# Performance work log

Hardware: AMD Instinct MI355X
Metric: run time of the kernel (lower is better)

The kernel has to match this reference:

```python
import jax, jax.numpy as jnp
import numpy as np

B, T, D, H = 2, 2048, 1024, 16
DH = D // H  # 64


def setup_inputs() -> dict:
    key = jax.random.key(0)
    ks = jax.random.split(key, 11)
    s = 1.0 / np.sqrt(D)
    return {
        "q": jax.random.normal(ks[0], (B, T, D), jnp.float32),
        "k": jax.random.normal(ks[1], (B, T, D), jnp.float32),
        "v": jax.random.normal(ks[2], (B, T, D), jnp.float32),
        "Wq": jax.random.normal(ks[3], (D, D), jnp.float32) * s,
        "bq": jnp.zeros((D,), jnp.float32),
        "Wk": jax.random.normal(ks[4], (D, D), jnp.float32) * s,
        "bk": jnp.zeros((D,), jnp.float32),
        "Wv": jax.random.normal(ks[5], (D, D), jnp.float32) * s,
        "bv": jnp.zeros((D,), jnp.float32),
        "Wo": jax.random.normal(ks[6], (D, D), jnp.float32) * s,
        "bo": jnp.zeros((D,), jnp.float32),
    }


def reference(q, k, v, Wq, bq, Wk, bk, Wv, bv, Wo, bo):
    Bq, Tq, _ = q.shape
    Tk = k.shape[1]
    # projections, split heads: [B, H, T, DH]
    qh = (q @ Wq + bq).reshape(Bq, Tq, H, DH).transpose(0, 2, 1, 3)
    kh = (k @ Wk + bk).reshape(Bq, Tk, H, DH).transpose(0, 2, 1, 3)
    vh = (v @ Wv + bv).reshape(Bq, Tk, H, DH).transpose(0, 2, 1, 3)
    # scores [B, H, Tq, Tk]
    scores = jnp.einsum("bhqd,bhkd->bhqk", qh, kh) / np.sqrt(DH)
    # causal mask with diagonal offset Tk - Tq (matches torch.tril semantics)
    ii = jnp.arange(Tq)[:, None]
    jj = jnp.arange(Tk)[None, :]
    causal = jj <= ii + (Tk - Tq)
    scores = jnp.where(causal, scores, -jnp.inf)
    attn = jax.nn.softmax(scores, axis=-1)
    x = jnp.einsum("bhqk,bhkd->bhqd", attn, vh)  # [B, H, Tq, DH]
    x = x.transpose(0, 2, 1, 3).reshape(Bq, Tq, H * DH)
    return x @ Wo + bo
```

## Files before the change

### kernel.cpp

```cpp
#include <hip/hip_runtime.h>

typedef unsigned short u16;
typedef unsigned int   u32;
typedef __attribute__((ext_vector_type(8)))  short short8;
typedef __attribute__((ext_vector_type(4)))  float f32x4;
typedef __attribute__((ext_vector_type(16))) float f32x16;
typedef __attribute__((ext_vector_type(2)))  u32 uint2v;
typedef __attribute__((ext_vector_type(4)))  u32 uint4v;

#define DEV __device__ __forceinline__

DEV u16 f2bf(float f) {
    u32 u = __builtin_bit_cast(u32, f);
    return (u16)((u + 0x7fffu + ((u >> 16) & 1u)) >> 16);
}
DEV float bf2f(u32 u) { return __builtin_bit_cast(float, u << 16); }
DEV u32 cvtpk(float a, float b) {
    u32 r;
    asm("v_cvt_pk_bf16_f32 %0, %1, %2" : "=v"(r) : "v"(a), "v"(b));
    return r;
}
typedef const __attribute__((address_space(1))) u32 g_u32;
typedef __attribute__((address_space(3))) u32 l_u32;
DEV void gload16(const u16* g, u16* l) {
    __builtin_amdgcn_global_load_lds((g_u32*)g, (l_u32*)l, 16, 0, 0);
}


template<int OMODE>
DEV void gemm_body(const u16* __restrict__ A_, const u16* __restrict__ Bt,
                   const float* __restrict__ bias, float oscale, void* C_) {
    constexpr int Kd = 1024;
    const int m0 = blockIdx.y * 128, n0 = blockIdx.x * 128;
    const int t = threadIdx.x, lane = t & 63, w = t >> 6;
    const int wm = w >> 1, wn = w & 1;
    const int l15 = lane & 15, l4 = lane >> 4;
    __shared__ __align__(16) u16 As[128 * 32];
    __shared__ __align__(16) u16 Bs[128 * 32];
    f32x4 acc[4][4] = {};

    for (int k0 = 0; k0 < Kd; k0 += 32) {
        #pragma unroll
        for (int rnd = 0; rnd < 2; rnd++) {
            int cc = rnd * 256 + t, row = cc >> 2, slot = cc & 3;
            gload16(Bt + (size_t)(n0 + row) * Kd + k0 + slot * 8, Bs + cc * 8);
            gload16(A_ + (size_t)(m0 + row) * Kd + k0 + slot * 8, As + cc * 8);
        }
        __syncthreads();
        short8 af[4], bfr[4];
        #pragma unroll
        for (int i = 0; i < 4; i++) {
            af[i]  = *(const short8*)(As + (wm * 64 + i * 16 + l15) * 32 + l4 * 8);
            bfr[i] = *(const short8*)(Bs + (wn * 64 + i * 16 + l15) * 32 + l4 * 8);
        }
        #pragma unroll
        for (int i = 0; i < 4; i++)
            #pragma unroll
            for (int j = 0; j < 4; j++)
                acc[i][j] = __builtin_amdgcn_mfma_f32_16x16x32_bf16(af[i], bfr[j], acc[i][j], 0, 0, 0);
        __syncthreads();
    }

    #pragma unroll
    for (int i = 0; i < 4; i++) {
        #pragma unroll
        for (int j = 0; j < 4; j++) {
            int col = n0 + wn * 64 + j * 16 + l15;
            int mb  = m0 + wm * 64 + i * 16 + l4 * 4;
            float bv = bias[col];
            if (OMODE == 2) {
                float* C = (float*)C_;
                #pragma unroll
                for (int r = 0; r < 4; r++)
                    C[(size_t)(mb + r) * 1024 + col] = acc[i][j][r] + bv;
            } else if (OMODE == 0) {
                u16* C = (u16*)C_;
                #pragma unroll
                for (int r = 0; r < 4; r++)
                    C[(size_t)(mb + r) * 1024 + col] = f2bf((acc[i][j][r] + bv) * oscale);
            } else if (OMODE == 3) {
                u16* C = (u16*)C_;
                int hh = col >> 6, dd = col & 63;
                int bb = mb >> 11, tt = mb & 2047;
                size_t tile = ((size_t)(bb * 16 + hh) * 64 + (tt >> 5)) * 2048;
                int c = dd >> 4, hi2 = (dd >> 3) & 1, e = dd & 7;
                int lob = tt & 31;
                #pragma unroll
                for (int r = 0; r < 4; r++)
                    C[tile + (size_t)((c * 2 + hi2) * 32 + lob + r) * 8 + e] =
                        f2bf(acc[i][j][r] + bv);
            } else {
                u16* C = (u16*)C_;
                int hh = col >> 6, dd = col & 63;
                int bb = mb >> 11, tt = mb & 2047;
                size_t tile = ((size_t)(bb * 16 + hh) * 64 + (tt >> 5)) * 2048;
                int tin = tt & 31, kc = tin >> 4, hi2 = (tin >> 3) & 1, e0 = tin & 7;
                int c2 = dd >> 5, lo2 = dd & 31;
                size_t off = tile + (size_t)((kc * 2 + c2) * 64 + hi2 * 32 + lo2) * 8 + e0;
                uint2v pp;
                pp[0] = cvtpk(acc[i][j][0] + bv, acc[i][j][1] + bv);
                pp[1] = cvtpk(acc[i][j][2] + bv, acc[i][j][3] + bv);
                *(uint2v*)(C + off) = pp;
            }
        }
    }
}

__global__ __launch_bounds__(256) void k_transw(const float* Wq, const float* Wk,
                                                const float* Wv, const float* Wo, u16* Wt) {
    int z = blockIdx.z;
    const float* W = z == 0 ? Wq : z == 1 ? Wk : z == 2 ? Wv : Wo;
    u16* O = Wt + (size_t)z * 1048576;
    __shared__ float tile[32][33];
    int n0 = blockIdx.x * 32, k0 = blockIdx.y * 32;
    int tx = threadIdx.x, ty = threadIdx.y;
    #pragma unroll
    for (int i = 0; i < 32; i += 8) tile[ty + i][tx] = W[(size_t)(k0 + ty + i) * 1024 + n0 + tx];
    __syncthreads();
    #pragma unroll
    for (int i = 0; i < 32; i += 8) O[(size_t)(n0 + ty + i) * 1024 + k0 + tx] = f2bf(tile[tx][ty + i]);
}

__global__ __launch_bounds__(256) void k_cvt(const float* q, const float* k, const float* v,
                                             u16* Abf) {
    int z = blockIdx.z;
    const float* src = z == 0 ? q : z == 1 ? k : v;
    u16* dst = Abf + (size_t)z * 4194304;
    size_t i = ((size_t)blockIdx.x * 256 + threadIdx.x) * 8;
    float4 a = *(const float4*)(src + i);
    float4 b = *(const float4*)(src + i + 4);
    uint4v o;
    o[0] = cvtpk(a.x, a.y); o[1] = cvtpk(a.z, a.w);
    o[2] = cvtpk(b.x, b.y); o[3] = cvtpk(b.z, b.w);
    *(uint4v*)(dst + i) = o;
}

__global__ __launch_bounds__(256) void k_proj(const u16* Abf, const u16* Wt,
                                              const float* bq, const float* bk,
                                              const float* bv, u16* QKV) {
    int z = blockIdx.z;
    if (z == 2)
        gemm_body<1>(Abf + (size_t)2 * 4194304, Wt + (size_t)2 * 1048576, bv, 1.f,
                     QKV + (size_t)2 * 4194304);
    else if (z == 1)
        gemm_body<3>(Abf + (size_t)4194304, Wt + (size_t)1048576, bk, 1.f,
                     QKV + (size_t)4194304);
    else
        gemm_body<0>(Abf, Wt, bq, 0.125f, QKV);
}

__global__ __launch_bounds__(256) void k_combine(const u16* Xp, const float* Lp, u16* Xc) {
    size_t idx = (size_t)blockIdx.x * 256 + threadIdx.x;
    size_t e = idx * 8;
    int row = (int)(e >> 10), hh = ((int)e & 1023) >> 6;
    float l0 = Lp[(size_t)row * 16 + hh];
    float l1 = Lp[65536 + (size_t)row * 16 + hh];
    float s = 1.0f / (l0 + l1);
    float w0 = l0 * s, w1 = l1 * s;
    uint4v x0 = *(const uint4v*)(Xp + e);
    uint4v x1 = *(const uint4v*)(Xp + (size_t)4194304 + e);
    uint4v o;
    #pragma unroll
    for (int j = 0; j < 4; j++) {
        float a0 = bf2f(x0[j] & 0xffffu) * w0 + bf2f(x1[j] & 0xffffu) * w1;
        float a1 = bf2f(x0[j] >> 16)    * w0 + bf2f(x1[j] >> 16)    * w1;
        o[j] = cvtpk(a0, a1);
    }
    *(uint4v*)(Xc + e) = o;
}

__global__ __launch_bounds__(256) void k_gemm_out(const u16* Xc, const u16* Wt,
                                                  const float* bo, float* out) {
    gemm_body<2>(Xc, Wt, bo, 1.f, out);
}

__global__ __launch_bounds__(256, 3) void k_attn(const u16* __restrict__ Qp,
                                                 const u16* __restrict__ Kp2,
                                                 const u16* __restrict__ Vp2,
                                                 u16* __restrict__ Xp, float* __restrict__ Lp) {
    const int bh = blockIdx.y, b = bh >> 4, h = bh & 15;
    const int t = threadIdx.x, lane = t & 63, w = t >> 6;
    const int lo = lane & 31, hi = lane >> 5;
    const int split = blockIdx.z;
    const int q0w = (int)(gridDim.x - 1 - blockIdx.x) * 128 + w * 32;
    const u16* Qb = Qp + (size_t)(b * 2048) * 1024 + h * 64;
    const u16* Kb = Kp2 + (size_t)bh * 64 * 2048;
    const u16* Vb = Vp2 + (size_t)bh * 64 * 2048;

    short8 qf[4];
    #pragma unroll
    for (int c = 0; c < 4; c++)
        qf[c] = *(const short8*)(Qb + (size_t)(q0w + lo) * 1024 + c * 16 + hi * 8);

    f32x16 O0 = {}, O1 = {};
    float lsum = 0.f;
    const int qg = q0w + lo;
    const int nk = (q0w >> 5) + 1;
    const int c0 = (nk + 1) >> 1;
    const int kbeg = split ? (c0 << 5) : 0;
    const int kend = split ? (nk << 5) : (c0 << 5);

#define LOADKV(KF, VF, kk) do {                                                          \
        const u16* kt_ = Kb + (size_t)((kk) >> 5) * 2048;                                \
        const u16* vt_ = Vb + (size_t)((kk) >> 5) * 2048;                                \
        _Pragma("unroll")                                                                \
        for (int c = 0; c < 4; c++)                                                      \
            KF[c] = *(const short8*)(kt_ + c * 512 + lane * 8);                          \
        _Pragma("unroll")                                                                \
        for (int j = 0; j < 4; j++)                                                      \
            VF[j] = *(const short8*)(vt_ + j * 512 + lane * 8);                          \
    } while (0)

#define COMPUTE(KF, VF, kk) do {                                                          \
        f32x16 S = {};                                                                    \
        _Pragma("unroll")                                                                 \
        for (int c = 0; c < 4; c++)                                                       \
            S = __builtin_amdgcn_mfma_f32_32x32x16_bf16(KF[c], qf[c], S, 0, 0, 0);        \
        const bool diag = ((kk) == q0w);                                                  \
        _Pragma("unroll")                                                                 \
        for (int kc = 0; kc < 2; kc++) {                                                  \
            float p[8];                                                                   \
            _Pragma("unroll")                                                             \
            for (int j = 0; j < 8; j++) {                                                 \
                int r = kc * 8 + j;                                                       \
                float s = S[r];                                                           \
                if (diag) {                                                               \
                    int kg = (kk) + (r & 3) + 8 * (r >> 2) + 4 * hi;                      \
                    s = (kg <= qg) ? s : -1e30f;                                          \
                }                                                                         \
                p[j] = __expf(s);                                                         \
            }                                                                             \
            lsum += (((p[0] + p[1]) + (p[2] + p[3])) + ((p[4] + p[5]) + (p[6] + p[7])));  \
            u32 w0 = cvtpk(p[0], p[1]), w1 = cvtpk(p[2], p[3]);                           \
            u32 w2 = cvtpk(p[4], p[5]), w3 = cvtpk(p[6], p[7]);                           \
            auto r0 = __builtin_amdgcn_permlane32_swap(w0, w2, false, false);             \
            auto r1 = __builtin_amdgcn_permlane32_swap(w1, w3, false, false);             \
            uint4v fw; fw[0] = r0[0]; fw[1] = r1[0]; fw[2] = r0[1]; fw[3] = r1[1];        \
            short8 pf = __builtin_bit_cast(short8, fw);                                   \
            O0 = __builtin_amdgcn_mfma_f32_32x32x16_bf16(pf, VF[kc * 2 + 0], O0, 0, 0, 0);\
            O1 = __builtin_amdgcn_mfma_f32_32x32x16_bf16(pf, VF[kc * 2 + 1], O1, 0, 0, 0);\
        }                                                                                 \
    } while (0)

    if (kbeg < kend) {
        short8 kf0[4], vf0[4], kf1[4], vf1[4];
        LOADKV(kf0, vf0, kbeg);
        int k0 = kbeg;
        while (true) {
            if (k0 + 32 < kend) LOADKV(kf1, vf1, k0 + 32);
            COMPUTE(kf0, vf0, k0);
            k0 += 32;
            if (k0 >= kend) break;
            if (k0 + 32 < kend) LOADKV(kf0, vf0, k0 + 32);
            COMPUTE(kf1, vf1, k0);
            k0 += 32;
            if (k0 >= kend) break;
        }
    }
#undef LOADKV
#undef COMPUTE

    float ltot = lsum + __shfl_xor(lsum, 32, 64);
    u16* Xb = Xp + (size_t)split * 4194304;
    #pragma unroll
    for (int r = 0; r < 16; r++) {
        int qr = (r & 3) + 8 * (r >> 2) + 4 * hi;
        float lt = __shfl(ltot, qr, 64);
        float linv = lt > 0.f ? 1.f / lt : 0.f;
        size_t rowb = (size_t)(b * 2048 + q0w + qr) * 1024 + h * 64;
        Xb[rowb + lo]      = f2bf(O0[r] * linv);
        Xb[rowb + 32 + lo] = f2bf(O1[r] * linv);
    }
    if (hi == 0)
        Lp[(size_t)split * 65536 + (size_t)(b * 2048 + q0w + lo) * 16 + h] = ltot;
}

extern "C" void kernel_launch(void* const* d_in, const int* in_sizes, int n_in,
                              void* d_out, int out_size, void* d_ws, size_t ws_size,
                              hipStream_t stream) {
    (void)in_sizes; (void)n_in; (void)out_size; (void)ws_size;
    const float* q  = (const float*)d_in[0];
    const float* k  = (const float*)d_in[1];
    const float* v  = (const float*)d_in[2];
    const float* Wq = (const float*)d_in[3];
    const float* bq = (const float*)d_in[4];
    const float* Wk = (const float*)d_in[5];
    const float* bk = (const float*)d_in[6];
    const float* Wv = (const float*)d_in[7];
    const float* bv = (const float*)d_in[8];
    const float* Wo = (const float*)d_in[9];
    const float* bo = (const float*)d_in[10];

    u16*   Wt  = (u16*)d_ws;
    u16*   QKV = Wt + (size_t)4 * 1048576;
    u16*   Abf = QKV + (size_t)3 * 4194304;
    u16*   Xp  = Abf;
    u16*   Xc  = Abf + (size_t)2 * 4194304;
    float* Lp  = (float*)(Abf + (size_t)3 * 4194304);

    k_transw<<<dim3(32, 32, 4), dim3(32, 8), 0, stream>>>(Wq, Wk, Wv, Wo, Wt);
    k_cvt<<<dim3(2048, 1, 3), 256, 0, stream>>>(q, k, v, Abf);
    k_proj<<<dim3(8, 32, 3), 256, 0, stream>>>(Abf, Wt, bq, bk, bv, QKV);
    k_attn<<<dim3(16, 32, 2), 256, 0, stream>>>(QKV, QKV + (size_t)4194304,
                                                QKV + (size_t)2 * 4194304, Xp, Lp);
    k_combine<<<2048, 256, 0, stream>>>(Xp, Lp, Xc);
    k_gemm_out<<<dim3(8, 32), 256, 0, stream>>>(Xc, Wt + (size_t)3 * 1048576,
                                                bo, (float*)d_out);
}
```

Before: 139.4 us.

## Pair causal query tiles per wave to balance work and drop split-K combine

Each wave now processes two mirrored 32-row query tiles (p and 63-p), so every wave does the same total number of key tiles under the causal mask. The key/value fragments are loaded once and shared by both tiles. This replaces the two-way key split, so the partial outputs, the Lp row sums and the k_combine kernel are no longer needed. In exchange the grid shrinks from 1024 to 256 blocks, launch bounds are lowered to one block, and register use roughly doubles because of the extra accumulators, which can reduce occupancy and latency hiding.

After: 134.0 us. 1.04x faster.

```diff
diff --git a/kernel.cpp b/kernel.cpp
--- a/kernel.cpp
+++ b/kernel.cpp
@@ -149,60 +149,39 @@
         gemm_body<0>(Abf, Wt, bq, 0.125f, QKV);
 }
 
-__global__ __launch_bounds__(256) void k_combine(const u16* Xp, const float* Lp, u16* Xc) {
-    size_t idx = (size_t)blockIdx.x * 256 + threadIdx.x;
-    size_t e = idx * 8;
-    int row = (int)(e >> 10), hh = ((int)e & 1023) >> 6;
-    float l0 = Lp[(size_t)row * 16 + hh];
-    float l1 = Lp[65536 + (size_t)row * 16 + hh];
-    float s = 1.0f / (l0 + l1);
-    float w0 = l0 * s, w1 = l1 * s;
-    uint4v x0 = *(const uint4v*)(Xp + e);
-    uint4v x1 = *(const uint4v*)(Xp + (size_t)4194304 + e);
-    uint4v o;
-    #pragma unroll
-    for (int j = 0; j < 4; j++) {
-        float a0 = bf2f(x0[j] & 0xffffu) * w0 + bf2f(x1[j] & 0xffffu) * w1;
-        float a1 = bf2f(x0[j] >> 16)    * w0 + bf2f(x1[j] >> 16)    * w1;
-        o[j] = cvtpk(a0, a1);
-    }
-    *(uint4v*)(Xc + e) = o;
-}
-
 __global__ __launch_bounds__(256) void k_gemm_out(const u16* Xc, const u16* Wt,
                                                   const float* bo, float* out) {
     gemm_body<2>(Xc, Wt, bo, 1.f, out);
 }
 
-__global__ __launch_bounds__(256, 3) void k_attn(const u16* __restrict__ Qp,
+__global__ __launch_bounds__(256, 1) void k_attn(const u16* __restrict__ Qp,
                                                  const u16* __restrict__ Kp2,
                                                  const u16* __restrict__ Vp2,
-                                                 u16* __restrict__ Xp, float* __restrict__ Lp) {
+                                                 u16* __restrict__ Xc) {
     const int bh = blockIdx.y, b = bh >> 4, h = bh & 15;
     const int t = threadIdx.x, lane = t & 63, w = t >> 6;
     const int lo = lane & 31, hi = lane >> 5;
-    const int split = blockIdx.z;
-    const int q0w = (int)(gridDim.x - 1 - blockIdx.x) * 128 + w * 32;
+    const int p = blockIdx.x * 4 + w;
+    const int q0a = p * 32, q0b = (63 - p) * 32;
+    const int nka = p + 1, nkb = 64 - p;
     const u16* Qb = Qp + (size_t)(b * 2048) * 1024 + h * 64;
     const u16* Kb = Kp2 + (size_t)bh * 64 * 2048;
     const u16* Vb = Vp2 + (size_t)bh * 64 * 2048;
 
-    short8 qf[4];
+    short8 qfa[4], qfb[4];
     #pragma unroll
-    for (int c = 0; c < 4; c++)
-        qf[c] = *(const short8*)(Qb + (size_t)(q0w + lo) * 1024 + c * 16 + hi * 8);
-
-    f32x16 O0 = {}, O1 = {};
-    float lsum = 0.f;
-    const int qg = q0w + lo;
-    const int nk = (q0w >> 5) + 1;
-    const int c0 = (nk + 1) >> 1;
-    const int kbeg = split ? (c0 << 5) : 0;
-    const int kend = split ? (nk << 5) : (c0 << 5);
-
-#define LOADKV(KF, VF, kk) do {                                                          \
-        const u16* kt_ = Kb + (size_t)((kk) >> 5) * 2048;                                \
-        const u16* vt_ = Vb + (size_t)((kk) >> 5) * 2048;                                \
+    for (int c = 0; c < 4; c++) {
+        qfa[c] = *(const short8*)(Qb + (size_t)(q0a + lo) * 1024 + c * 16 + hi * 8);
+        qfb[c] = *(const short8*)(Qb + (size_t)(q0b + lo) * 1024 + c * 16 + hi * 8);
+    }
+
+    f32x16 Oa0 = {}, Oa1 = {}, Ob0 = {}, Ob1 = {};
+    float lsa = 0.f, lsb = 0.f;
+    const int qga = q0a + lo, qgb = q0b + lo;
+
+#define LOADKV(KF, VF, kt) do {                                                          \
+        const u16* kt_ = Kb + (size_t)(kt) * 2048;                                       \
+        const u16* vt_ = Vb + (size_t)(kt) * 2048;                                       \
         _Pragma("unroll")                                                                \
         for (int c = 0; c < 4; c++)                                                      \
             KF[c] = *(const short8*)(kt_ + c * 512 + lane * 8);                          \
@@ -211,28 +190,24 @@
             VF[j] = *(const short8*)(vt_ + j * 512 + lane * 8);                          \
     } while (0)
 
-#define COMPUTE(KF, VF, kk) do {                                                          \
-        f32x16 S = {};                                                                    \
-        _Pragma("unroll")                                                                 \
-        for (int c = 0; c < 4; c++)                                                       \
-            S = __builtin_amdgcn_mfma_f32_32x32x16_bf16(KF[c], qf[c], S, 0, 0, 0);        \
-        const bool diag = ((kk) == q0w);                                                  \
+#define SMPV(S, O0, O1, lsum, diag, qg, kt, VF) do {                                      \
         _Pragma("unroll")                                                                 \
         for (int kc = 0; kc < 2; kc++) {                                                  \
-            float p[8];                                                                   \
+            float pv[8];                                                                  \
             _Pragma("unroll")                                                             \
             for (int j = 0; j < 8; j++) {                                                 \
                 int r = kc * 8 + j;                                                       \
                 float s = S[r];                                                           \
                 if (diag) {                                                               \
-                    int kg = (kk) + (r & 3) + 8 * (r >> 2) + 4 * hi;                      \
-                    s = (kg <= qg) ? s : -1e30f;                                          \
+                    int kg = (kt) * 32 + (r & 3) + 8 * (r >> 2) + 4 * hi;                 \
+                    s = (kg <= (qg)) ? s : -1e30f;                                        \
                 }                                                                         \
-                p[j] = __expf(s);                                                         \
+                pv[j] = __expf(s);                                                        \
             }                                                                             \
-            lsum += (((p[0] + p[1]) + (p[2] + p[3])) + ((p[4] + p[5]) + (p[6] + p[7])));  \
-            u32 w0 = cvtpk(p[0], p[1]), w1 = cvtpk(p[2], p[3]);                           \
-            u32 w2 = cvtpk(p[4], p[5]), w3 = cvtpk(p[6], p[7]);                           \
+            lsum += (((pv[0] + pv[1]) + (pv[2] + pv[3])) +                                \
+                     ((pv[4] + pv[5]) + (pv[6] + pv[7])));                                \
+            u32 w0 = cvtpk(pv[0], pv[1]), w1 = cvtpk(pv[2], pv[3]);                       \
+            u32 w2 = cvtpk(pv[4], pv[5]), w3 = cvtpk(pv[6], pv[7]);                       \
             auto r0 = __builtin_amdgcn_permlane32_swap(w0, w2, false, false);             \
             auto r1 = __builtin_amdgcn_permlane32_swap(w1, w3, false, false);             \
             uint4v fw; fw[0] = r0[0]; fw[1] = r1[0]; fw[2] = r0[1]; fw[3] = r1[1];        \
@@ -242,37 +217,56 @@
         }                                                                                 \
     } while (0)
 
-    if (kbeg < kend) {
+#define STEP(KF, VF, kt) do {                                                             \
+        const bool doA = (kt) < nka;                                                      \
+        f32x16 Sb = {}, Sa = {};                                                          \
+        _Pragma("unroll")                                                                 \
+        for (int c = 0; c < 4; c++)                                                       \
+            Sb = __builtin_amdgcn_mfma_f32_32x32x16_bf16(KF[c], qfb[c], Sb, 0, 0, 0);     \
+        if (doA) {                                                                        \
+            _Pragma("unroll")                                                             \
+            for (int c = 0; c < 4; c++)                                                   \
+                Sa = __builtin_amdgcn_mfma_f32_32x32x16_bf16(KF[c], qfa[c], Sa, 0, 0, 0); \
+            SMPV(Sa, Oa0, Oa1, lsa, (kt) == nka - 1, qga, kt, VF);                        \
+        }                                                                                 \
+        SMPV(Sb, Ob0, Ob1, lsb, (kt) == nkb - 1, qgb, kt, VF);                            \
+    } while (0)
+
+    {
         short8 kf0[4], vf0[4], kf1[4], vf1[4];
-        LOADKV(kf0, vf0, kbeg);
-        int k0 = kbeg;
+        LOADKV(kf0, vf0, 0);
+        int kt = 0;
         while (true) {
-            if (k0 + 32 < kend) LOADKV(kf1, vf1, k0 + 32);
-            COMPUTE(kf0, vf0, k0);
-            k0 += 32;
-            if (k0 >= kend) break;
-            if (k0 + 32 < kend) LOADKV(kf0, vf0, k0 + 32);
-            COMPUTE(kf1, vf1, k0);
-            k0 += 32;
-            if (k0 >= kend) break;
+            if (kt + 1 < nkb) LOADKV(kf1, vf1, kt + 1);
+            STEP(kf0, vf0, kt);
+            ++kt;
+            if (kt >= nkb) break;
+            if (kt + 1 < nkb) LOADKV(kf0, vf0, kt + 1);
+            STEP(kf1, vf1, kt);
+            ++kt;
+            if (kt >= nkb) break;
         }
     }
 #undef LOADKV
-#undef COMPUTE
-
-    float ltot = lsum + __shfl_xor(lsum, 32, 64);
-    u16* Xb = Xp + (size_t)split * 4194304;
-    #pragma unroll
-    for (int r = 0; r < 16; r++) {
-        int qr = (r & 3) + 8 * (r >> 2) + 4 * hi;
-        float lt = __shfl(ltot, qr, 64);
-        float linv = lt > 0.f ? 1.f / lt : 0.f;
-        size_t rowb = (size_t)(b * 2048 + q0w + qr) * 1024 + h * 64;
-        Xb[rowb + lo]      = f2bf(O0[r] * linv);
-        Xb[rowb + 32 + lo] = f2bf(O1[r] * linv);
-    }
-    if (hi == 0)
-        Lp[(size_t)split * 65536 + (size_t)(b * 2048 + q0w + lo) * 16 + h] = ltot;
+#undef SMPV
+#undef STEP
+
+#define EPI(O0, O1, lsum, q0) do {                                                        \
+        float ltot = (lsum) + __shfl_xor((lsum), 32, 64);                                 \
+        _Pragma("unroll")                                                                 \
+        for (int r = 0; r < 16; r++) {                                                    \
+            int qr = (r & 3) + 8 * (r >> 2) + 4 * hi;                                     \
+            float lt = __shfl(ltot, qr, 64);                                              \
+            float linv = lt > 0.f ? 1.f / lt : 0.f;                                       \
+            size_t rowb = (size_t)(b * 2048 + (q0) + qr) * 1024 + h * 64;                 \
+            Xc[rowb + lo]      = f2bf(O0[r] * linv);                                      \
+            Xc[rowb + 32 + lo] = f2bf(O1[r] * linv);                                      \
+        }                                                                                 \
+    } while (0)
+
+    EPI(Oa0, Oa1, lsa, q0a);
+    EPI(Ob0, Ob1, lsb, q0b);
+#undef EPI
 }
 
 extern "C" void kernel_launch(void* const* d_in, const int* in_sizes, int n_in,
@@ -291,19 +285,16 @@
     const float* Wo = (const float*)d_in[9];
     const float* bo = (const float*)d_in[10];
 
-    u16*   Wt  = (u16*)d_ws;
-    u16*   QKV = Wt + (size_t)4 * 1048576;
-    u16*   Abf = QKV + (size_t)3 * 4194304;
-    u16*   Xp  = Abf;
-    u16*   Xc  = Abf + (size_t)2 * 4194304;
-    float* Lp  = (float*)(Abf + (size_t)3 * 4194304);
+    u16* Wt  = (u16*)d_ws;
+    u16* QKV = Wt + (size_t)4 * 1048576;
+    u16* Abf = QKV + (size_t)3 * 4194304;
+    u16* Xc  = Abf;
 
     k_transw<<<dim3(32, 32, 4), dim3(32, 8), 0, stream>>>(Wq, Wk, Wv, Wo, Wt);
     k_cvt<<<dim3(2048, 1, 3), 256, 0, stream>>>(q, k, v, Abf);
     k_proj<<<dim3(8, 32, 3), 256, 0, stream>>>(Abf, Wt, bq, bk, bv, QKV);
-    k_attn<<<dim3(16, 32, 2), 256, 0, stream>>>(QKV, QKV + (size_t)4194304,
-                                                QKV + (size_t)2 * 4194304, Xp, Lp);
-    k_combine<<<2048, 256, 0, stream>>>(Xp, Lp, Xc);
+    k_attn<<<dim3(8, 32), 256, 0, stream>>>(QKV, QKV + (size_t)4194304,
+                                            QKV + (size_t)2 * 4194304, Xc);
     k_gemm_out<<<dim3(8, 32), 256, 0, stream>>>(Xc, Wt + (size_t)3 * 1048576,
                                                 bo, (float*)d_out);
 }
```

## Share K/V tiles via LDS double buffering and drop split-K combine pass

Applied to the files above, without the earlier changes.

The attention kernel no longer splits the key range into two halves that a separate combine kernel merges. Each block now stages K/V tiles into double-buffered shared memory with async global-to-LDS loads, so its four waves share one copy instead of each reading K/V from global memory. The log2(e) factor is folded into the Q projection scale so exp2 can replace exp. In exchange the grid is half as large, occupancy drops to 2 blocks per CU, and per-tile __syncthreads are added while waves with shorter causal ranges sit idle.

After: 143.0 us. +2.6%, slower.

```diff
diff --git a/kernel.cpp b/kernel.cpp
--- a/kernel.cpp
+++ b/kernel.cpp
@@ -146,27 +146,7 @@
         gemm_body<3>(Abf + (size_t)4194304, Wt + (size_t)1048576, bk, 1.f,
                      QKV + (size_t)4194304);
     else
-        gemm_body<0>(Abf, Wt, bq, 0.125f, QKV);
-}
-
-__global__ __launch_bounds__(256) void k_combine(const u16* Xp, const float* Lp, u16* Xc) {
-    size_t idx = (size_t)blockIdx.x * 256 + threadIdx.x;
-    size_t e = idx * 8;
-    int row = (int)(e >> 10), hh = ((int)e & 1023) >> 6;
-    float l0 = Lp[(size_t)row * 16 + hh];
-    float l1 = Lp[65536 + (size_t)row * 16 + hh];
-    float s = 1.0f / (l0 + l1);
-    float w0 = l0 * s, w1 = l1 * s;
-    uint4v x0 = *(const uint4v*)(Xp + e);
-    uint4v x1 = *(const uint4v*)(Xp + (size_t)4194304 + e);
-    uint4v o;
-    #pragma unroll
-    for (int j = 0; j < 4; j++) {
-        float a0 = bf2f(x0[j] & 0xffffu) * w0 + bf2f(x1[j] & 0xffffu) * w1;
-        float a1 = bf2f(x0[j] >> 16)    * w0 + bf2f(x1[j] >> 16)    * w1;
-        o[j] = cvtpk(a0, a1);
-    }
-    *(uint4v*)(Xc + e) = o;
+        gemm_body<0>(Abf, Wt, bq, 0.125f * 1.44269504088896f, QKV);
 }
 
 __global__ __launch_bounds__(256) void k_gemm_out(const u16* Xc, const u16* Wt,
@@ -174,105 +154,94 @@
     gemm_body<2>(Xc, Wt, bo, 1.f, out);
 }
 
-__global__ __launch_bounds__(256, 3) void k_attn(const u16* __restrict__ Qp,
+__global__ __launch_bounds__(256, 2) void k_attn(const u16* __restrict__ Qp,
                                                  const u16* __restrict__ Kp2,
                                                  const u16* __restrict__ Vp2,
-                                                 u16* __restrict__ Xp, float* __restrict__ Lp) {
+                                                 u16* __restrict__ Xc) {
     const int bh = blockIdx.y, b = bh >> 4, h = bh & 15;
     const int t = threadIdx.x, lane = t & 63, w = t >> 6;
     const int lo = lane & 31, hi = lane >> 5;
-    const int split = blockIdx.z;
-    const int q0w = (int)(gridDim.x - 1 - blockIdx.x) * 128 + w * 32;
+    const int j = 15 - (int)blockIdx.x;
+    const int q0 = (j * 4 + w) * 32;
+    const int NTw = j * 4 + w + 1;
+    const int NT  = j * 4 + 4;
     const u16* Qb = Qp + (size_t)(b * 2048) * 1024 + h * 64;
     const u16* Kb = Kp2 + (size_t)bh * 64 * 2048;
     const u16* Vb = Vp2 + (size_t)bh * 64 * 2048;
 
+    __shared__ __align__(16) u16 Ks[2][2048];
+    __shared__ __align__(16) u16 Vs[2][2048];
+
     short8 qf[4];
     #pragma unroll
     for (int c = 0; c < 4; c++)
-        qf[c] = *(const short8*)(Qb + (size_t)(q0w + lo) * 1024 + c * 16 + hi * 8);
+        qf[c] = *(const short8*)(Qb + (size_t)(q0 + lo) * 1024 + c * 16 + hi * 8);
 
     f32x16 O0 = {}, O1 = {};
     float lsum = 0.f;
-    const int qg = q0w + lo;
-    const int nk = (q0w >> 5) + 1;
-    const int c0 = (nk + 1) >> 1;
-    const int kbeg = split ? (c0 << 5) : 0;
-    const int kend = split ? (nk << 5) : (c0 << 5);
-
-#define LOADKV(KF, VF, kk) do {                                                          \
-        const u16* kt_ = Kb + (size_t)((kk) >> 5) * 2048;                                \
-        const u16* vt_ = Vb + (size_t)((kk) >> 5) * 2048;                                \
-        _Pragma("unroll")                                                                \
-        for (int c = 0; c < 4; c++)                                                      \
-            KF[c] = *(const short8*)(kt_ + c * 512 + lane * 8);                          \
-        _Pragma("unroll")                                                                \
-        for (int j = 0; j < 4; j++)                                                      \
-            VF[j] = *(const short8*)(vt_ + j * 512 + lane * 8);                          \
+    const int qg = q0 + lo;
+
+#define STAGE(buf, kt) do {                                                              \
+        gload16(Kb + (size_t)(kt) * 2048 + t * 8, Ks[buf] + t * 8);                      \
+        gload16(Vb + (size_t)(kt) * 2048 + t * 8, Vs[buf] + t * 8);                      \
     } while (0)
 
-#define COMPUTE(KF, VF, kk) do {                                                          \
-        f32x16 S = {};                                                                    \
-        _Pragma("unroll")                                                                 \
-        for (int c = 0; c < 4; c++)                                                       \
-            S = __builtin_amdgcn_mfma_f32_32x32x16_bf16(KF[c], qf[c], S, 0, 0, 0);        \
-        const bool diag = ((kk) == q0w);                                                  \
-        _Pragma("unroll")                                                                 \
-        for (int kc = 0; kc < 2; kc++) {                                                  \
-            float p[8];                                                                   \
-            _Pragma("unroll")                                                             \
-            for (int j = 0; j < 8; j++) {                                                 \
-                int r = kc * 8 + j;                                                       \
-                float s = S[r];                                                           \
-                if (diag) {                                                               \
-                    int kg = (kk) + (r & 3) + 8 * (r >> 2) + 4 * hi;                      \
-                    s = (kg <= qg) ? s : -1e30f;                                          \
-                }                                                                         \
-                p[j] = __expf(s);                                                         \
-            }                                                                             \
-            lsum += (((p[0] + p[1]) + (p[2] + p[3])) + ((p[4] + p[5]) + (p[6] + p[7])));  \
-            u32 w0 = cvtpk(p[0], p[1]), w1 = cvtpk(p[2], p[3]);                           \
-            u32 w2 = cvtpk(p[4], p[5]), w3 = cvtpk(p[6], p[7]);                           \
-            auto r0 = __builtin_amdgcn_permlane32_swap(w0, w2, false, false);             \
-            auto r1 = __builtin_amdgcn_permlane32_swap(w1, w3, false, false);             \
-            uint4v fw; fw[0] = r0[0]; fw[1] = r1[0]; fw[2] = r0[1]; fw[3] = r1[1];        \
-            short8 pf = __builtin_bit_cast(short8, fw);                                   \
-            O0 = __builtin_amdgcn_mfma_f32_32x32x16_bf16(pf, VF[kc * 2 + 0], O0, 0, 0, 0);\
-            O1 = __builtin_amdgcn_mfma_f32_32x32x16_bf16(pf, VF[kc * 2 + 1], O1, 0, 0, 0);\
-        }                                                                                 \
-    } while (0)
-
-    if (kbeg < kend) {
-        short8 kf0[4], vf0[4], kf1[4], vf1[4];
-        LOADKV(kf0, vf0, kbeg);
-        int k0 = kbeg;
-        while (true) {
-            if (k0 + 32 < kend) LOADKV(kf1, vf1, k0 + 32);
-            COMPUTE(kf0, vf0, k0);
-            k0 += 32;
-            if (k0 >= kend) break;
-            if (k0 + 32 < kend) LOADKV(kf0, vf0, k0 + 32);
-            COMPUTE(kf1, vf1, k0);
-            k0 += 32;
-            if (k0 >= kend) break;
-        }
-    }
-#undef LOADKV
-#undef COMPUTE
+    STAGE(0, 0);
+    for (int kt = 0; kt < NT; kt++) {
+        __syncthreads();
+        if (kt + 1 < NT) STAGE((kt + 1) & 1, kt + 1);
+        if (kt < NTw) {
+            const u16* kl = Ks[kt & 1];
+            const u16* vl = Vs[kt & 1];
+            short8 kf[4], vf[4];
+            #pragma unroll
+            for (int c = 0; c < 4; c++) {
+                kf[c] = *(const short8*)(kl + (c * 64 + lane) * 8);
+                vf[c] = *(const short8*)(vl + (c * 64 + lane) * 8);
+            }
+            f32x16 S = {};
+            #pragma unroll
+            for (int c = 0; c < 4; c++)
+                S = __builtin_amdgcn_mfma_f32_32x32x16_bf16(kf[c], qf[c], S, 0, 0, 0);
+            const bool diag = (kt == NTw - 1);
+            #pragma unroll
+            for (int kc = 0; kc < 2; kc++) {
+                float pv[8];
+                #pragma unroll
+                for (int jj = 0; jj < 8; jj++) {
+                    int r = kc * 8 + jj;
+                    float s = S[r];
+                    if (diag) {
+                        int kg = kt * 32 + (r & 3) + 8 * (r >> 2) + 4 * hi;
+                        s = (kg <= qg) ? s : -1e30f;
+                    }
+                    pv[jj] = __builtin_amdgcn_exp2f(s);
+                }
+                lsum += (((pv[0] + pv[1]) + (pv[2] + pv[3])) +
+                         ((pv[4] + pv[5]) + (pv[6] + pv[7])));
+                u32 w0 = cvtpk(pv[0], pv[1]), w1 = cvtpk(pv[2], pv[3]);
+                u32 w2 = cvtpk(pv[4], pv[5]), w3 = cvtpk(pv[6], pv[7]);
+                auto r0 = __builtin_amdgcn_permlane32_swap(w0, w2, false, false);
+                auto r1 = __builtin_amdgcn_permlane32_swap(w1, w3, false, false);
+                uint4v fw; fw[0] = r0[0]; fw[1] = r1[0]; fw[2] = r0[1]; fw[3] = r1[1];
+                short8 pf = __builtin_bit_cast(short8, fw);
+                O0 = __builtin_amdgcn_mfma_f32_32x32x16_bf16(pf, vf[kc * 2 + 0], O0, 0, 0, 0);
+                O1 = __builtin_amdgcn_mfma_f32_32x32x16_bf16(pf, vf[kc * 2 + 1], O1, 0, 0, 0);
+            }
+        }
+    }
+#undef STAGE
 
     float ltot = lsum + __shfl_xor(lsum, 32, 64);
-    u16* Xb = Xp + (size_t)split * 4194304;
     #pragma unroll
     for (int r = 0; r < 16; r++) {
         int qr = (r & 3) + 8 * (r >> 2) + 4 * hi;
         float lt = __shfl(ltot, qr, 64);
         float linv = lt > 0.f ? 1.f / lt : 0.f;
-        size_t rowb = (size_t)(b * 2048 + q0w + qr) * 1024 + h * 64;
-        Xb[rowb + lo]      = f2bf(O0[r] * linv);
-        Xb[rowb + 32 + lo] = f2bf(O1[r] * linv);
-    }
-    if (hi == 0)
-        Lp[(size_t)split * 65536 + (size_t)(b * 2048 + q0w + lo) * 16 + h] = ltot;
+        size_t rowb = (size_t)(b * 2048 + q0 + qr) * 1024 + h * 64;
+        Xc[rowb + lo]      = f2bf(O0[r] * linv);
+        Xc[rowb + 32 + lo] = f2bf(O1[r] * linv);
+    }
 }
 
 extern "C" void kernel_launch(void* const* d_in, const int* in_sizes, int n_in,
@@ -291,19 +260,16 @@
     const float* Wo = (const float*)d_in[9];
     const float* bo = (const float*)d_in[10];
 
-    u16*   Wt  = (u16*)d_ws;
-    u16*   QKV = Wt + (size_t)4 * 1048576;
-    u16*   Abf = QKV + (size_t)3 * 4194304;
-    u16*   Xp  = Abf;
-    u16*   Xc  = Abf + (size_t)2 * 4194304;
-    float* Lp  = (float*)(Abf + (size_t)3 * 4194304);
+    u16* Wt  = (u16*)d_ws;
+    u16* QKV = Wt + (size_t)4 * 1048576;
+    u16* Abf = QKV + (size_t)3 * 4194304;
+    u16* Xc  = Abf;
 
     k_transw<<<dim3(32, 32, 4), dim3(32, 8), 0, stream>>>(Wq, Wk, Wv, Wo, Wt);
     k_cvt<<<dim3(2048, 1, 3), 256, 0, stream>>>(q, k, v, Abf);
     k_proj<<<dim3(8, 32, 3), 256, 0, stream>>>(Abf, Wt, bq, bk, bv, QKV);
-    k_attn<<<dim3(16, 32, 2), 256, 0, stream>>>(QKV, QKV + (size_t)4194304,
-                                                QKV + (size_t)2 * 4194304, Xp, Lp);
-    k_combine<<<2048, 256, 0, stream>>>(Xp, Lp, Xc);
+    k_attn<<<dim3(16, 32), 256, 0, stream>>>(QKV, QKV + (size_t)4194304,
+                                             QKV + (size_t)2 * 4194304, Xc);
     k_gemm_out<<<dim3(8, 32), 256, 0, stream>>>(Xc, Wt + (size_t)3 * 1048576,
                                                 bo, (float*)d_out);
 }
```

## Split attention KV work three ways interleaved and balance query tiles across waves

Applied to the files above, without the earlier changes.

The attention kernel now splits each query tile's key blocks into three interleaved partitions (stride 3) instead of two contiguous halves. Each block's four waves take query tiles spaced 16 apart, which evens out causal work per block. Softmax uses exp2 with log2(e) folded into the Q projection scale. The combine kernel merges three partial outputs, and Xc is moved into the now-free QKV buffer. This costs more combine traffic and partial writes in exchange for better load balance and more parallelism.

Result: faster. 131.2 us (-5.9%).

```diff
diff --git a/kernel.cpp b/kernel.cpp
--- a/kernel.cpp
+++ b/kernel.cpp
@@ -146,7 +146,7 @@
         gemm_body<3>(Abf + (size_t)4194304, Wt + (size_t)1048576, bk, 1.f,
                      QKV + (size_t)4194304);
     else
-        gemm_body<0>(Abf, Wt, bq, 0.125f, QKV);
+        gemm_body<0>(Abf, Wt, bq, 0.125f * 1.44269504088896f, QKV);
 }
 
 __global__ __launch_bounds__(256) void k_combine(const u16* Xp, const float* Lp, u16* Xc) {
@@ -155,15 +155,19 @@
     int row = (int)(e >> 10), hh = ((int)e & 1023) >> 6;
     float l0 = Lp[(size_t)row * 16 + hh];
     float l1 = Lp[65536 + (size_t)row * 16 + hh];
-    float s = 1.0f / (l0 + l1);
-    float w0 = l0 * s, w1 = l1 * s;
+    float l2 = Lp[131072 + (size_t)row * 16 + hh];
+    float s = 1.0f / (l0 + l1 + l2);
+    float w0 = l0 * s, w1 = l1 * s, w2 = l2 * s;
     uint4v x0 = *(const uint4v*)(Xp + e);
     uint4v x1 = *(const uint4v*)(Xp + (size_t)4194304 + e);
+    uint4v x2 = *(const uint4v*)(Xp + (size_t)2 * 4194304 + e);
     uint4v o;
     #pragma unroll
     for (int j = 0; j < 4; j++) {
-        float a0 = bf2f(x0[j] & 0xffffu) * w0 + bf2f(x1[j] & 0xffffu) * w1;
-        float a1 = bf2f(x0[j] >> 16)    * w0 + bf2f(x1[j] >> 16)    * w1;
+        float a0 = bf2f(x0[j] & 0xffffu) * w0 + bf2f(x1[j] & 0xffffu) * w1
+                 + bf2f(x2[j] & 0xffffu) * w2;
+        float a1 = bf2f(x0[j] >> 16) * w0 + bf2f(x1[j] >> 16) * w1
+                 + bf2f(x2[j] >> 16) * w2;
         o[j] = cvtpk(a0, a1);
     }
     *(uint4v*)(Xc + e) = o;
@@ -181,8 +185,11 @@
     const int bh = blockIdx.y, b = bh >> 4, h = bh & 15;
     const int t = threadIdx.x, lane = t & 63, w = t >> 6;
     const int lo = lane & 31, hi = lane >> 5;
-    const int split = blockIdx.z;
-    const int q0w = (int)(gridDim.x - 1 - blockIdx.x) * 128 + w * 32;
+    const int par = blockIdx.z;
+    const int j = (int)blockIdx.x;
+    const int qt = w * 16 + j;
+    const int q0 = qt * 32;
+    const int NTw = qt + 1;
     const u16* Qb = Qp + (size_t)(b * 2048) * 1024 + h * 64;
     const u16* Kb = Kp2 + (size_t)bh * 64 * 2048;
     const u16* Vb = Vp2 + (size_t)bh * 64 * 2048;
@@ -190,49 +197,46 @@
     short8 qf[4];
     #pragma unroll
     for (int c = 0; c < 4; c++)
-        qf[c] = *(const short8*)(Qb + (size_t)(q0w + lo) * 1024 + c * 16 + hi * 8);
+        qf[c] = *(const short8*)(Qb + (size_t)(q0 + lo) * 1024 + c * 16 + hi * 8);
 
     f32x16 O0 = {}, O1 = {};
     float lsum = 0.f;
-    const int qg = q0w + lo;
-    const int nk = (q0w >> 5) + 1;
-    const int c0 = (nk + 1) >> 1;
-    const int kbeg = split ? (c0 << 5) : 0;
-    const int kend = split ? (nk << 5) : (c0 << 5);
-
-#define LOADKV(KF, VF, kk) do {                                                          \
-        const u16* kt_ = Kb + (size_t)((kk) >> 5) * 2048;                                \
-        const u16* vt_ = Vb + (size_t)((kk) >> 5) * 2048;                                \
+    const int qg = q0 + lo;
+
+#define LOADKV(KF, VF, kt) do {                                                          \
+        const u16* kt_ = Kb + (size_t)(kt) * 2048;                                       \
+        const u16* vt_ = Vb + (size_t)(kt) * 2048;                                       \
         _Pragma("unroll")                                                                \
         for (int c = 0; c < 4; c++)                                                      \
             KF[c] = *(const short8*)(kt_ + c * 512 + lane * 8);                          \
         _Pragma("unroll")                                                                \
-        for (int j = 0; j < 4; j++)                                                      \
-            VF[j] = *(const short8*)(vt_ + j * 512 + lane * 8);                          \
+        for (int jj = 0; jj < 4; jj++)                                                   \
+            VF[jj] = *(const short8*)(vt_ + jj * 512 + lane * 8);                        \
     } while (0)
 
-#define COMPUTE(KF, VF, kk) do {                                                          \
+#define COMPUTE(KF, VF, kt) do {                                                          \
         f32x16 S = {};                                                                    \
         _Pragma("unroll")                                                                 \
         for (int c = 0; c < 4; c++)                                                       \
             S = __builtin_amdgcn_mfma_f32_32x32x16_bf16(KF[c], qf[c], S, 0, 0, 0);        \
-        const bool diag = ((kk) == q0w);                                                  \
+        const bool diag = ((kt) == NTw - 1);                                              \
         _Pragma("unroll")                                                                 \
         for (int kc = 0; kc < 2; kc++) {                                                  \
-            float p[8];                                                                   \
+            float pv[8];                                                                  \
             _Pragma("unroll")                                                             \
-            for (int j = 0; j < 8; j++) {                                                 \
-                int r = kc * 8 + j;                                                       \
+            for (int jj = 0; jj < 8; jj++) {                                              \
+                int r = kc * 8 + jj;                                                      \
                 float s = S[r];                                                           \
                 if (diag) {                                                               \
-                    int kg = (kk) + (r & 3) + 8 * (r >> 2) + 4 * hi;                      \
+                    int kg = (kt) * 32 + (r & 3) + 8 * (r >> 2) + 4 * hi;                 \
                     s = (kg <= qg) ? s : -1e30f;                                          \
                 }                                                                         \
-                p[j] = __expf(s);                                                         \
+                pv[jj] = __builtin_amdgcn_exp2f(s);                                       \
             }                                                                             \
-            lsum += (((p[0] + p[1]) + (p[2] + p[3])) + ((p[4] + p[5]) + (p[6] + p[7])));  \
-            u32 w0 = cvtpk(p[0], p[1]), w1 = cvtpk(p[2], p[3]);                           \
-            u32 w2 = cvtpk(p[4], p[5]), w3 = cvtpk(p[6], p[7]);                           \
+            lsum += (((pv[0] + pv[1]) + (pv[2] + pv[3])) +                                \
+                     ((pv[4] + pv[5]) + (pv[6] + pv[7])));                                \
+            u32 w0 = cvtpk(pv[0], pv[1]), w1 = cvtpk(pv[2], pv[3]);                       \
+            u32 w2 = cvtpk(pv[4], pv[5]), w3 = cvtpk(pv[6], pv[7]);                       \
             auto r0 = __builtin_amdgcn_permlane32_swap(w0, w2, false, false);             \
             auto r1 = __builtin_amdgcn_permlane32_swap(w1, w3, false, false);             \
             uint4v fw; fw[0] = r0[0]; fw[1] = r1[0]; fw[2] = r0[1]; fw[3] = r1[1];        \
@@ -242,37 +246,39 @@
         }                                                                                 \
     } while (0)
 
-    if (kbeg < kend) {
+    {
         short8 kf0[4], vf0[4], kf1[4], vf1[4];
-        LOADKV(kf0, vf0, kbeg);
-        int k0 = kbeg;
-        while (true) {
-            if (k0 + 32 < kend) LOADKV(kf1, vf1, k0 + 32);
-            COMPUTE(kf0, vf0, k0);
-            k0 += 32;
-            if (k0 >= kend) break;
-            if (k0 + 32 < kend) LOADKV(kf0, vf0, k0 + 32);
-            COMPUTE(kf1, vf1, k0);
-            k0 += 32;
-            if (k0 >= kend) break;
+        int kt = par;
+        if (kt < NTw) {
+            LOADKV(kf0, vf0, kt);
+            while (true) {
+                if (kt + 3 < NTw) LOADKV(kf1, vf1, kt + 3);
+                COMPUTE(kf0, vf0, kt);
+                kt += 3;
+                if (kt >= NTw) break;
+                if (kt + 3 < NTw) LOADKV(kf0, vf0, kt + 3);
+                COMPUTE(kf1, vf1, kt);
+                kt += 3;
+                if (kt >= NTw) break;
+            }
         }
     }
 #undef LOADKV
 #undef COMPUTE
 
     float ltot = lsum + __shfl_xor(lsum, 32, 64);
-    u16* Xb = Xp + (size_t)split * 4194304;
+    u16* Xb = Xp + (size_t)par * 4194304;
     #pragma unroll
     for (int r = 0; r < 16; r++) {
         int qr = (r & 3) + 8 * (r >> 2) + 4 * hi;
         float lt = __shfl(ltot, qr, 64);
         float linv = lt > 0.f ? 1.f / lt : 0.f;
-        size_t rowb = (size_t)(b * 2048 + q0w + qr) * 1024 + h * 64;
+        size_t rowb = (size_t)(b * 2048 + q0 + qr) * 1024 + h * 64;
         Xb[rowb + lo]      = f2bf(O0[r] * linv);
         Xb[rowb + 32 + lo] = f2bf(O1[r] * linv);
     }
     if (hi == 0)
-        Lp[(size_t)split * 65536 + (size_t)(b * 2048 + q0w + lo) * 16 + h] = ltot;
+        Lp[(size_t)par * 65536 + (size_t)(b * 2048 + q0 + lo) * 16 + h] = ltot;
 }
 
 extern "C" void kernel_launch(void* const* d_in, const int* in_sizes, int n_in,
@@ -295,13 +301,13 @@
     u16*   QKV = Wt + (size_t)4 * 1048576;
     u16*   Abf = QKV + (size_t)3 * 4194304;
     u16*   Xp  = Abf;
-    u16*   Xc  = Abf + (size_t)2 * 4194304;
+    u16*   Xc  = QKV;
     float* Lp  = (float*)(Abf + (size_t)3 * 4194304);
 
     k_transw<<<dim3(32, 32, 4), dim3(32, 8), 0, stream>>>(Wq, Wk, Wv, Wo, Wt);
     k_cvt<<<dim3(2048, 1, 3), 256, 0, stream>>>(q, k, v, Abf);
     k_proj<<<dim3(8, 32, 3), 256, 0, stream>>>(Abf, Wt, bq, bk, bv, QKV);
-    k_attn<<<dim3(16, 32, 2), 256, 0, stream>>>(QKV, QKV + (size_t)4194304,
+    k_attn<<<dim3(16, 32, 3), 256, 0, stream>>>(QKV, QKV + (size_t)4194304,
                                                 QKV + (size_t)2 * 4194304, Xp, Lp);
     k_combine<<<2048, 256, 0, stream>>>(Xp, Lp, Xc);
     k_gemm_out<<<dim3(8, 32), 256, 0, stream>>>(Xc, Wt + (size_t)3 * 1048576,
```
